# Performance work log

Measured on AMD Instinct MI355X. Metric: run time of the kernel, lower is better.

Reference implementation:

```python
import jax, jax.numpy as jnp
import numpy as np

VOCAB, EDIM, HDIM, ODIM = 100000, 128, 128, 10
BN_EPS = 1e-3  # keras BatchNormalization default epsilon


def _bn(x, gamma, beta, axes):
    # training-mode batch norm (batch statistics), as in a Keras training step
    m = jnp.mean(x, axis=axes, keepdims=True)
    v = jnp.var(x, axis=axes, keepdims=True)
    return gamma * (x - m) * jax.lax.rsqrt(v + BN_EPS) + beta


def _lstm_last(x, mask, W, U, b):
    # Keras LSTM, gate order [i, f, c, o]; masked steps carry state through.
    # x: [B,T,E], mask: [B,T] bool. Returns final hidden state [B,H].
    B, T, _ = x.shape
    H = U.shape[0]
    xg = jnp.einsum('bte,eg->btg', x, W) + b  # precomputed input projections [B,T,4H]

    def step(carry, inp):
        h, c = carry
        g, m = inp                      # g: [B,4H], m: [B]
        g = g + h @ U
        i, f, cc, o = jnp.split(g, 4, axis=-1)
        c_new = jax.nn.sigmoid(f) * c + jax.nn.sigmoid(i) * jnp.tanh(cc)
        h_new = jax.nn.sigmoid(o) * jnp.tanh(c_new)
        m = m[:, None]
        return (jnp.where(m, h_new, h), jnp.where(m, c_new, c)), None

    init = (jnp.zeros((B, H), x.dtype), jnp.zeros((B, H), x.dtype))
    (h, _), _ = jax.lax.scan(step, init, (xg.transpose(1, 0, 2), mask.T))
    return h


def setup_inputs() -> dict:
    key = jax.random.key(0)
    ks = jax.random.split(key, 12)
    s = 0.05
    ids = jax.random.randint(ks[0], (128, 1024), 0, VOCAB)
    return {
        'ids': ids,
        'embed_table': jax.random.normal(ks[1], (VOCAB, EDIM), jnp.float32) * s,
        'gamma1': jnp.ones((EDIM,), jnp.float32),
        'beta1': jnp.zeros((EDIM,), jnp.float32),
        'Wf': jax.random.normal(ks[2], (EDIM, 4 * HDIM), jnp.float32) * s,
        'Uf': jax.random.normal(ks[3], (HDIM, 4 * HDIM), jnp.float32) * s,
        'bf': jnp.zeros((4 * HDIM,), jnp.float32),
        'Wb': jax.random.normal(ks[4], (EDIM, 4 * HDIM), jnp.float32) * s,
        'Ub': jax.random.normal(ks[5], (HDIM, 4 * HDIM), jnp.float32) * s,
        'bb': jnp.zeros((4 * HDIM,), jnp.float32),
        'gamma2': jnp.ones((2 * HDIM,), jnp.float32),
        'beta2': jnp.zeros((2 * HDIM,), jnp.float32),
        'Wd': jax.random.normal(ks[6], (2 * HDIM, ODIM), jnp.float32) * s,
        'bd': jnp.zeros((ODIM,), jnp.float32),
    }


def reference(ids, embed_table, gamma1, beta1, Wf, Uf, bf, Wb, Ub, bb,
              gamma2, beta2, Wd, bd):
    mask = ids != 0                              # mask_zero=True
    x = embed_table[ids]                         # [B,T,E]
    x = _bn(x, gamma1, beta1, axes=(0, 1))
    h_fwd = _lstm_last(x, mask, Wf, Uf, bf)      # forward direction
    h_bwd = _lstm_last(x[:, ::-1], mask[:, ::-1], Wb, Ub, bb)  # go_backwards
    h = jnp.concatenate([h_fwd, h_bwd], axis=-1)  # merge_mode='concat' -> [B,2H]
    h = _bn(h, gamma2, beta2, axes=(0,))
    return jax.nn.softmax(h @ Wd + bd, axis=-1)
```

## Files before the change

kernel.cpp:

```cpp
#include <hip/hip_runtime.h>
#include <hip/hip_bf16.h>
#include <stdint.h>

#define VOCAB  100000
#define EDIM   128
#define HDIM   128
#define T_LEN  1024
#define BATCH  128
#define GDIM   512
#define NROWS  (BATCH*T_LEN)
#define BN_EPS 1e-3f

using short8 = __attribute__((ext_vector_type(8))) short;
using f32x4  = __attribute__((ext_vector_type(4))) float;

#define WS_SCALE  0u
#define WS_SHIFT  512u
#define WS_PSUM   1024u
#define WS_PSQ    (WS_PSUM + 524288u)
#define WS_HCAT   (WS_PSQ + 524288u)
#define WS_FRAGS  (WS_HCAT + 131072u)
#define WS_XN     (WS_FRAGS + 524288u)

__device__ __forceinline__ short f2bf(float f) {
    uint32_t u = __float_as_uint(f);
    return (short)((u + 0x7fffu + ((u >> 16) & 1u)) >> 16);
}

#define LOG2E 1.4426950408889634f
__device__ __forceinline__ float sigm2(float x) {
    return __builtin_amdgcn_rcpf(1.f + exp2f(x * (-LOG2E)));
}
__device__ __forceinline__ float tanh2(float x) {
    return 1.f - 2.f * __builtin_amdgcn_rcpf(1.f + exp2f(x * (2.f * LOG2E)));
}

#define BAR() asm volatile("s_waitcnt lgkmcnt(0)\n\ts_barrier" ::: "memory")

__global__ void k_bn1_partial(const int* __restrict__ ids,
                              const float* __restrict__ tab,
                              float* __restrict__ psum, float* __restrict__ psq) {
    __shared__ float ls[256], lq[256];
    int f = threadIdx.x & 127, rr = threadIdx.x >> 7;
    int r0 = blockIdx.x * 128;
    float s = 0.f, q = 0.f;
    for (int r = rr; r < 128; r += 2) {
        int id = ids[r0 + r];
        float v = tab[(size_t)id * EDIM + f];
        s += v; q += v * v;
    }
    ls[threadIdx.x] = s; lq[threadIdx.x] = q;
    __syncthreads();
    if (threadIdx.x < 128) {
        psum[blockIdx.x * 128 + f] = ls[f] + ls[f + 128];
        psq [blockIdx.x * 128 + f] = lq[f] + lq[f + 128];
    }
}

__global__ void k_bn1_final(const float* __restrict__ psum, const float* __restrict__ psq,
                            const float* __restrict__ gamma, const float* __restrict__ beta,
                            float* __restrict__ scale, float* __restrict__ shift) {
    int f = threadIdx.x;
    float s = 0.f, q = 0.f;
    for (int p = 0; p < 1024; ++p) { s += psum[p * 128 + f]; q += psq[p * 128 + f]; }
    const float inv_n = 1.0f / (float)NROWS;
    float m  = s * inv_n;
    float v  = q * inv_n - m * m;
    float sc = gamma[f] * rsqrtf(v + BN_EPS);
    scale[f] = sc;
    shift[f] = beta[f] - m * sc;
}

__global__ void k_embed_norm(const int* __restrict__ ids,
                             const float* __restrict__ tab,
                             const float* __restrict__ scale,
                             const float* __restrict__ shift,
                             short* __restrict__ xn) {
    int gid = blockIdx.x * blockDim.x + threadIdx.x;
    int row = gid >> 4, seg = gid & 15;
    int id  = ids[row];
    const float* src = tab + (size_t)id * EDIM + seg * 8;
    short8 out;
#pragma unroll
    for (int j = 0; j < 8; ++j) {
        float v = scale[seg * 8 + j] * src[j] + shift[seg * 8 + j];
        out[j] = f2bf(v);
    }
    *(short8*)(xn + (size_t)row * EDIM + seg * 8) = out;
}

__global__ void k_prepack(const float* __restrict__ Wf, const float* __restrict__ Uf,
                          const float* __restrict__ Wb, const float* __restrict__ Ub,
                          short* __restrict__ frags) {
    int gid = blockIdx.x * blockDim.x + threadIdx.x;
    int l  = gid & 63;
    int f  = (gid >> 6) & 31;
    int w  = (gid >> 11) & 7;
    int d  = gid >> 14;
    int s    = f >> 4;
    int gate = (f >> 2) & 3;
    int kc   = f & 3;
    const float* M = s ? (d ? Ub : Uf) : (d ? Wb : Wf);
    int rbase = 32 * kc + 8 * (l >> 4);
    int col   = 128 * gate + 16 * w + (l & 15);
    short8 out;
#pragma unroll
    for (int j = 0; j < 8; ++j) out[j] = f2bf(M[(size_t)(rbase + j) * GDIM + col]);
    *(short8*)(frags + (size_t)gid * 8) = out;
}

#define MFMA(A, B, C) __builtin_amdgcn_mfma_f32_16x16x32_bf16((A), (B), (C), 0, 0, 0)
#define S8(x) __builtin_bit_cast(short8, x)

__global__ void __launch_bounds__(512, 2)
k_lstm(const int* __restrict__ ids,
       const short* __restrict__ xn,
       const short* __restrict__ frags,
       const float* __restrict__ bf_, const float* __restrict__ bb_,
       float* __restrict__ hcat) {
    const int d   = blockIdx.x >> 7;
    const int b   = blockIdx.x & 127;
    const int tid = threadIdx.x;
    const int w   = tid >> 6, l = tid & 63, g = l >> 4, li = l & 15;

    __shared__ float xg_lds[2][16][512];
    __shared__ __align__(16) short h_s[2][HDIM];
    __shared__ unsigned char m_s[T_LEN];

    const short8* wsrc = (const short8*)frags + (size_t)(d * 8 + w) * 32 * 64 + l;

    short8 u00 = wsrc[(16+0)*64],  u01 = wsrc[(16+1)*64],  u02 = wsrc[(16+2)*64],  u03 = wsrc[(16+3)*64];
    short8 u10 = wsrc[(16+4)*64],  u11 = wsrc[(16+5)*64],  u12 = wsrc[(16+6)*64],  u13 = wsrc[(16+7)*64];
    short8 u20 = wsrc[(16+8)*64],  u21 = wsrc[(16+9)*64],  u22 = wsrc[(16+10)*64], u23 = wsrc[(16+11)*64];
    short8 u30 = wsrc[(16+12)*64], u31 = wsrc[(16+13)*64], u32 = wsrc[(16+14)*64], u33 = wsrc[(16+15)*64];

    short8 wq00 = wsrc[0*64],  wq01 = wsrc[1*64],  wq02 = wsrc[2*64],  wq03 = wsrc[3*64];
    short8 wq10 = wsrc[4*64],  wq11 = wsrc[5*64],  wq12 = wsrc[6*64],  wq13 = wsrc[7*64];
    short8 wq20 = wsrc[8*64],  wq21 = wsrc[9*64],  wq22 = wsrc[10*64], wq23 = wsrc[11*64];
    short8 wq30 = wsrc[12*64], wq31 = wsrc[13*64], wq32 = wsrc[14*64], wq33 = wsrc[15*64];

    const float* bias = d ? bb_ : bf_;
    const float bia0 = bias[0*128 + w*16 + li];
    const float bia1 = bias[1*128 + w*16 + li];
    const float bia2 = bias[2*128 + w*16 + li];
    const float bia3 = bias[3*128 + w*16 + li];

    {
        const int* idrow = ids + b * T_LEN;
        m_s[tid]       = idrow[tid] != 0;
        m_s[tid + 512] = idrow[tid + 512] != 0;
    }
    if (tid < HDIM) h_s[0][tid] = 0;
    float c_reg = 0.f, h_reg = 0.f;

    float* const xgw = &xg_lds[0][0][0] + w * 16 + li;

    uint4 ga0, ga1, ga2, ga3;
#define GATHER(C_) { \
        int s0_ = 16 * (C_) + li; \
        int p_  = d ? (T_LEN - 1 - s0_) : s0_; \
        const uint4* gb_ = (const uint4*)xn + (size_t)(b * T_LEN + p_) * 16; \
        ga0 = gb_[g]; ga1 = gb_[4 + g]; ga2 = gb_[8 + g]; ga3 = gb_[12 + g]; \
    }

#define XWGATE(GG, W0, W1, W2, W3, BIA, XGBASE) { \
        f32x4 ax = {(BIA), (BIA), (BIA), (BIA)}; \
        ax = MFMA(S8(ga0), W0, ax); \
        ax = MFMA(S8(ga1), W1, ax); \
        ax = MFMA(S8(ga2), W2, ax); \
        ax = MFMA(S8(ga3), W3, ax); \
        float* dst_ = (XGBASE) + (GG) * 128; \
        dst_[(4*g+0)*512] = ax[0]; dst_[(4*g+1)*512] = ax[1]; \
        dst_[(4*g+2)*512] = ax[2]; dst_[(4*g+3)*512] = ax[3]; \
    }

    GATHER(0);
    XWGATE(0, wq00, wq01, wq02, wq03, bia0, xgw);
    XWGATE(1, wq10, wq11, wq12, wq13, bia1, xgw);
    XWGATE(2, wq20, wq21, wq22, wq23, bia2, xgw);
    XWGATE(3, wq30, wq31, wq32, wq33, bia3, xgw);
    __syncthreads();

    float xa0, xa1, xa2, xa3, xb0, xb1, xb2, xb3;
    int   ma, mb;
    xa0 = xgw[0]; xa1 = xgw[128]; xa2 = xgw[256]; xa3 = xgw[384];
    ma  = m_s[d ? (T_LEN - 1) : 0];

    f32x4 a0 = {0.f,0.f,0.f,0.f}, a1 = {0.f,0.f,0.f,0.f};
    f32x4 a2 = {0.f,0.f,0.f,0.f}, a3 = {0.f,0.f,0.f,0.f};

#define STEP(J, XC0, XC1, XC2, XC3, XN0, XN1, XN2, XN3, MC, MN) { \
        const uint4* hp_ = (const uint4*)(h_s[(J) & 1]); \
        uint4 hf0 = hp_[g], hf1 = hp_[4 + g], hf2 = hp_[8 + g], hf3 = hp_[12 + g]; \
        a0[0] = (XC0); a1[0] = (XC1); a2[0] = (XC2); a3[0] = (XC3); \
        if (c < 63) { \
            if ((J) == 4) { wq00 = wsrc[0*64];  wq01 = wsrc[1*64];  wq02 = wsrc[2*64];  wq03 = wsrc[3*64];  } \
            if ((J) == 5) { wq10 = wsrc[4*64];  wq11 = wsrc[5*64];  wq12 = wsrc[6*64];  wq13 = wsrc[7*64];  } \
            if ((J) == 6) { wq20 = wsrc[8*64];  wq21 = wsrc[9*64];  wq22 = wsrc[10*64]; wq23 = wsrc[11*64]; } \
            if ((J) == 7) { wq30 = wsrc[12*64]; wq31 = wsrc[13*64]; wq32 = wsrc[14*64]; wq33 = wsrc[15*64]; } \
            if ((J) == 8)  XWGATE(0, wq00, wq01, wq02, wq03, bia0, xgw + ((c + 1) & 1) * 8192); \
            if ((J) == 9)  XWGATE(1, wq10, wq11, wq12, wq13, bia1, xgw + ((c + 1) & 1) * 8192); \
            if ((J) == 10) XWGATE(2, wq20, wq21, wq22, wq23, bia2, xgw + ((c + 1) & 1) * 8192); \
            if ((J) == 11) XWGATE(3, wq30, wq31, wq32, wq33, bia3, xgw + ((c + 1) & 1) * 8192); \
        } \
        a0 = MFMA(S8(hf0), u00, a0); a1 = MFMA(S8(hf0), u10, a1); \
        a2 = MFMA(S8(hf0), u20, a2); a3 = MFMA(S8(hf0), u30, a3); \
        a0 = MFMA(S8(hf1), u01, a0); a1 = MFMA(S8(hf1), u11, a1); \
        a2 = MFMA(S8(hf1), u21, a2); a3 = MFMA(S8(hf1), u31, a3); \
        a0 = MFMA(S8(hf2), u02, a0); a1 = MFMA(S8(hf2), u12, a1); \
        a2 = MFMA(S8(hf2), u22, a2); a3 = MFMA(S8(hf2), u32, a3); \
        a0 = MFMA(S8(hf3), u03, a0); a1 = MFMA(S8(hf3), u13, a1); \
        a2 = MFMA(S8(hf3), u23, a2); a3 = MFMA(S8(hf3), u33, a3); \
        if (!((c == 63) && ((J) == 15))) { \
            const float* rb_ = xgw + (((J) < 15) ? (c & 1) : ((c + 1) & 1)) * 8192 \
                                   + (((J) + 1) & 15) * 512; \
            XN0 = rb_[0]; XN1 = rb_[128]; XN2 = rb_[256]; XN3 = rb_[384]; \
            int sn_ = c * 16 + (J) + 1; \
            MN = m_s[d ? (T_LEN - 1 - sn_) : sn_]; \
        } \
        { \
            float gi = a0[0], gf = a1[0], gc = a2[0], go = a3[0]; \
            float si = sigm2(gi); \
            float sf = sigm2(gf); \
            float so = sigm2(go); \
            float tc = tanh2(gc); \
            float cn = sf * c_reg + si * tc; \
            float th = tanh2(cn); \
            float hn = so * th; \
            if (MC) { c_reg = cn; h_reg = hn; } \
            if (l < 16) h_s[((J) + 1) & 1][w * 16 + li] = f2bf(h_reg); \
        } \
        BAR(); \
    }

#pragma unroll 1
    for (int c = 0; c < 64; ++c) {
        if (c < 63) GATHER(c + 1);
        STEP(0,  xa0, xa1, xa2, xa3, xb0, xb1, xb2, xb3, ma, mb)
        STEP(1,  xb0, xb1, xb2, xb3, xa0, xa1, xa2, xa3, mb, ma)
        STEP(2,  xa0, xa1, xa2, xa3, xb0, xb1, xb2, xb3, ma, mb)
        STEP(3,  xb0, xb1, xb2, xb3, xa0, xa1, xa2, xa3, mb, ma)
        STEP(4,  xa0, xa1, xa2, xa3, xb0, xb1, xb2, xb3, ma, mb)
        STEP(5,  xb0, xb1, xb2, xb3, xa0, xa1, xa2, xa3, mb, ma)
        STEP(6,  xa0, xa1, xa2, xa3, xb0, xb1, xb2, xb3, ma, mb)
        STEP(7,  xb0, xb1, xb2, xb3, xa0, xa1, xa2, xa3, mb, ma)
        STEP(8,  xa0, xa1, xa2, xa3, xb0, xb1, xb2, xb3, ma, mb)
        STEP(9,  xb0, xb1, xb2, xb3, xa0, xa1, xa2, xa3, mb, ma)
        STEP(10, xa0, xa1, xa2, xa3, xb0, xb1, xb2, xb3, ma, mb)
        STEP(11, xb0, xb1, xb2, xb3, xa0, xa1, xa2, xa3, mb, ma)
        STEP(12, xa0, xa1, xa2, xa3, xb0, xb1, xb2, xb3, ma, mb)
        STEP(13, xb0, xb1, xb2, xb3, xa0, xa1, xa2, xa3, mb, ma)
        STEP(14, xa0, xa1, xa2, xa3, xb0, xb1, xb2, xb3, ma, mb)
        STEP(15, xb0, xb1, xb2, xb3, xa0, xa1, xa2, xa3, mb, ma)
    }

    if (l < 16) hcat[b * 256 + d * 128 + w * 16 + li] = h_reg;
}

__global__ void k_head(const float* __restrict__ hcat,
                       const float* __restrict__ gamma2, const float* __restrict__ beta2,
                       const float* __restrict__ Wd, const float* __restrict__ bd,
                       float* __restrict__ out) {
    __shared__ float sc_s[256], sh_s[256];
    __shared__ float logits[BATCH * 10];
    int tid = threadIdx.x;
    if (tid < 256) {
        float s = 0.f, q = 0.f;
        for (int bb = 0; bb < BATCH; ++bb) { float v = hcat[bb * 256 + tid]; s += v; q += v * v; }
        float m  = s / (float)BATCH;
        float v  = q / (float)BATCH - m * m;
        float sc = gamma2[tid] * rsqrtf(v + BN_EPS);
        sc_s[tid] = sc;
        sh_s[tid] = beta2[tid] - m * sc;
    }
    __syncthreads();
    {
        int bb = tid >> 3, oq = tid & 7;
        float acc0 = bd[oq], acc1 = (oq < 2) ? bd[8 + oq] : 0.f;
        for (int k = 0; k < 256; ++k) {
            float hv = sc_s[k] * hcat[bb * 256 + k] + sh_s[k];
            acc0 += hv * Wd[k * 10 + oq];
            if (oq < 2) acc1 += hv * Wd[k * 10 + 8 + oq];
        }
        logits[bb * 10 + oq] = acc0;
        if (oq < 2) logits[bb * 10 + 8 + oq] = acc1;
    }
    __syncthreads();
    if (tid < BATCH) {
        float lm = -1e30f;
#pragma unroll
        for (int o = 0; o < 10; ++o) lm = fmaxf(lm, logits[tid * 10 + o]);
        float e[10], s = 0.f;
#pragma unroll
        for (int o = 0; o < 10; ++o) { e[o] = __expf(logits[tid * 10 + o] - lm); s += e[o]; }
        float inv = __builtin_amdgcn_rcpf(s);
#pragma unroll
        for (int o = 0; o < 10; ++o) out[tid * 10 + o] = e[o] * inv;
    }
}

extern "C" void kernel_launch(void* const* d_in, const int* in_sizes, int n_in,
                              void* d_out, int out_size, void* d_ws, size_t ws_size,
                              hipStream_t stream) {
    const int*   ids = (const int*)  d_in[0];
    const float* tab = (const float*)d_in[1];
    const float* g1  = (const float*)d_in[2];
    const float* b1  = (const float*)d_in[3];
    const float* Wf  = (const float*)d_in[4];
    const float* Uf  = (const float*)d_in[5];
    const float* bfv = (const float*)d_in[6];
    const float* Wb  = (const float*)d_in[7];
    const float* Ub  = (const float*)d_in[8];
    const float* bbv = (const float*)d_in[9];
    const float* g2  = (const float*)d_in[10];
    const float* b2  = (const float*)d_in[11];
    const float* Wd  = (const float*)d_in[12];
    const float* bd  = (const float*)d_in[13];

    char*  ws    = (char*)d_ws;
    float* scale = (float*)(ws + WS_SCALE);
    float* shift = (float*)(ws + WS_SHIFT);
    float* psum  = (float*)(ws + WS_PSUM);
    float* psq   = (float*)(ws + WS_PSQ);
    float* hcat  = (float*)(ws + WS_HCAT);
    short* fragp = (short*)(ws + WS_FRAGS);
    short* xnp   = (short*)(ws + WS_XN);

    k_bn1_partial<<<1024, 256, 0, stream>>>(ids, tab, psum, psq);
    k_bn1_final  <<<1, 128, 0, stream>>>(psum, psq, g1, b1, scale, shift);
    k_embed_norm <<<8192, 256, 0, stream>>>(ids, tab, scale, shift, xnp);
    k_prepack    <<<128, 256, 0, stream>>>(Wf, Uf, Wb, Ub, fragp);
    k_lstm       <<<256, 512, 0, stream>>>(ids, xnp, fragp, bfv, bbv, hcat);
    k_head       <<<1, 1024, 0, stream>>>(hcat, g2, b2, Wd, bd, (float*)d_out);
}
```

Measured before the change: 678.4 us.

## Fold activation scales into LSTM weights, split MFMA chains, bit-pack masks

Pre-scales the gate weights and biases by -log2e (or 2log2e for the cell gate) during prepacking, so each sigmoid and tanh becomes a bare exp2 plus reciprocal. The recurrent MFMA chain is split into two independent accumulator chains, and the input projection is added after the MFMAs rather than seeded into them, which shortens the serial dependency on each step. Masks move from per-step LDS bytes to 64-bit ballot words built by a new kernel and read once per 16-step chunk. The xg LDS layout is made gate-interleaved so one vector load replaces four scalar loads, the per-chunk reload of W fragments is dropped, and bf16 conversion uses v_cvt_pk_bf16_f32. Rounding of the scaled weights to bf16 changes numerics slightly, and the mask words reuse the psum workspace region, which is safe only because the partial sums are consumed before the new kernel runs.

```diff
diff --git a/kernel.cpp b/kernel.cpp
--- a/kernel.cpp
+++ b/kernel.cpp
@@ -22,17 +22,12 @@
 #define WS_FRAGS  (WS_HCAT + 131072u)
 #define WS_XN     (WS_FRAGS + 524288u)
 
+#define SGI_K (-1.4426950408889634f)
+#define SGC_K ( 2.8853900817779268f)
+
 __device__ __forceinline__ short f2bf(float f) {
     uint32_t u = __float_as_uint(f);
     return (short)((u + 0x7fffu + ((u >> 16) & 1u)) >> 16);
-}
-
-#define LOG2E 1.4426950408889634f
-__device__ __forceinline__ float sigm2(float x) {
-    return __builtin_amdgcn_rcpf(1.f + exp2f(x * (-LOG2E)));
-}
-__device__ __forceinline__ float tanh2(float x) {
-    return 1.f - 2.f * __builtin_amdgcn_rcpf(1.f + exp2f(x * (2.f * LOG2E)));
 }
 
 #define BAR() asm volatile("s_waitcnt lgkmcnt(0)\n\ts_barrier" ::: "memory")
@@ -71,6 +66,12 @@
     shift[f] = beta[f] - m * sc;
 }
 
+__global__ void k_packmask(const int* __restrict__ ids, unsigned long long* __restrict__ mwords) {
+    int gid = blockIdx.x * 1024 + threadIdx.x;
+    unsigned long long bal = __ballot(ids[gid] != 0);
+    if ((threadIdx.x & 63) == 0) mwords[gid >> 6] = bal;
+}
+
 __global__ void k_embed_norm(const int* __restrict__ ids,
                              const float* __restrict__ tab,
                              const float* __restrict__ scale,
@@ -101,11 +102,12 @@
     int gate = (f >> 2) & 3;
     int kc   = f & 3;
     const float* M = s ? (d ? Ub : Uf) : (d ? Wb : Wf);
+    const float gs = (gate == 2) ? SGC_K : SGI_K;
     int rbase = 32 * kc + 8 * (l >> 4);
     int col   = 128 * gate + 16 * w + (l & 15);
     short8 out;
 #pragma unroll
-    for (int j = 0; j < 8; ++j) out[j] = f2bf(M[(size_t)(rbase + j) * GDIM + col]);
+    for (int j = 0; j < 8; ++j) out[j] = f2bf(gs * M[(size_t)(rbase + j) * GDIM + col]);
     *(short8*)(frags + (size_t)gid * 8) = out;
 }
 
@@ -113,9 +115,9 @@
 #define S8(x) __builtin_bit_cast(short8, x)
 
 __global__ void __launch_bounds__(512, 2)
-k_lstm(const int* __restrict__ ids,
-       const short* __restrict__ xn,
+k_lstm(const short* __restrict__ xn,
        const short* __restrict__ frags,
+       const unsigned long long* __restrict__ mwords,
        const float* __restrict__ bf_, const float* __restrict__ bb_,
        float* __restrict__ hcat) {
     const int d   = blockIdx.x >> 7;
@@ -125,35 +127,32 @@
 
     __shared__ float xg_lds[2][16][512];
     __shared__ __align__(16) short h_s[2][HDIM];
-    __shared__ unsigned char m_s[T_LEN];
+
+    float* const xgf = &xg_lds[0][0][0];
+    float* const xgr = xgf + (w * 16 + li) * 4;
 
     const short8* wsrc = (const short8*)frags + (size_t)(d * 8 + w) * 32 * 64 + l;
+
+    short8 wq00 = wsrc[0*64],  wq01 = wsrc[1*64],  wq02 = wsrc[2*64],  wq03 = wsrc[3*64];
+    short8 wq10 = wsrc[4*64],  wq11 = wsrc[5*64],  wq12 = wsrc[6*64],  wq13 = wsrc[7*64];
+    short8 wq20 = wsrc[8*64],  wq21 = wsrc[9*64],  wq22 = wsrc[10*64], wq23 = wsrc[11*64];
+    short8 wq30 = wsrc[12*64], wq31 = wsrc[13*64], wq32 = wsrc[14*64], wq33 = wsrc[15*64];
 
     short8 u00 = wsrc[(16+0)*64],  u01 = wsrc[(16+1)*64],  u02 = wsrc[(16+2)*64],  u03 = wsrc[(16+3)*64];
     short8 u10 = wsrc[(16+4)*64],  u11 = wsrc[(16+5)*64],  u12 = wsrc[(16+6)*64],  u13 = wsrc[(16+7)*64];
     short8 u20 = wsrc[(16+8)*64],  u21 = wsrc[(16+9)*64],  u22 = wsrc[(16+10)*64], u23 = wsrc[(16+11)*64];
     short8 u30 = wsrc[(16+12)*64], u31 = wsrc[(16+13)*64], u32 = wsrc[(16+14)*64], u33 = wsrc[(16+15)*64];
 
-    short8 wq00 = wsrc[0*64],  wq01 = wsrc[1*64],  wq02 = wsrc[2*64],  wq03 = wsrc[3*64];
-    short8 wq10 = wsrc[4*64],  wq11 = wsrc[5*64],  wq12 = wsrc[6*64],  wq13 = wsrc[7*64];
-    short8 wq20 = wsrc[8*64],  wq21 = wsrc[9*64],  wq22 = wsrc[10*64], wq23 = wsrc[11*64];
-    short8 wq30 = wsrc[12*64], wq31 = wsrc[13*64], wq32 = wsrc[14*64], wq33 = wsrc[15*64];
-
     const float* bias = d ? bb_ : bf_;
-    const float bia0 = bias[0*128 + w*16 + li];
-    const float bia1 = bias[1*128 + w*16 + li];
-    const float bia2 = bias[2*128 + w*16 + li];
-    const float bia3 = bias[3*128 + w*16 + li];
-
-    {
-        const int* idrow = ids + b * T_LEN;
-        m_s[tid]       = idrow[tid] != 0;
-        m_s[tid + 512] = idrow[tid + 512] != 0;
-    }
+    const float bia0 = bias[0*128 + w*16 + li] * SGI_K;
+    const float bia1 = bias[1*128 + w*16 + li] * SGI_K;
+    const float bia2 = bias[2*128 + w*16 + li] * SGC_K;
+    const float bia3 = bias[3*128 + w*16 + li] * SGI_K;
+
     if (tid < HDIM) h_s[0][tid] = 0;
     float c_reg = 0.f, h_reg = 0.f;
 
-    float* const xgw = &xg_lds[0][0][0] + w * 16 + li;
+    const f32x4 Z = {0.f, 0.f, 0.f, 0.f};
 
     uint4 ga0, ga1, ga2, ga3;
 #define GATHER(C_) { \
@@ -163,72 +162,76 @@
         ga0 = gb_[g]; ga1 = gb_[4 + g]; ga2 = gb_[8 + g]; ga3 = gb_[12 + g]; \
     }
 
-#define XWGATE(GG, W0, W1, W2, W3, BIA, XGBASE) { \
+#define XWGATE(GG, W0, W1, W2, W3, BIA, BUF) { \
         f32x4 ax = {(BIA), (BIA), (BIA), (BIA)}; \
         ax = MFMA(S8(ga0), W0, ax); \
         ax = MFMA(S8(ga1), W1, ax); \
         ax = MFMA(S8(ga2), W2, ax); \
         ax = MFMA(S8(ga3), W3, ax); \
-        float* dst_ = (XGBASE) + (GG) * 128; \
+        float* dst_ = xgf + (BUF) * 8192 + (w * 16 + li) * 4 + (GG); \
         dst_[(4*g+0)*512] = ax[0]; dst_[(4*g+1)*512] = ax[1]; \
         dst_[(4*g+2)*512] = ax[2]; dst_[(4*g+3)*512] = ax[3]; \
     }
 
     GATHER(0);
-    XWGATE(0, wq00, wq01, wq02, wq03, bia0, xgw);
-    XWGATE(1, wq10, wq11, wq12, wq13, bia1, xgw);
-    XWGATE(2, wq20, wq21, wq22, wq23, bia2, xgw);
-    XWGATE(3, wq30, wq31, wq32, wq33, bia3, xgw);
+    XWGATE(0, wq00, wq01, wq02, wq03, bia0, 0);
+    XWGATE(1, wq10, wq11, wq12, wq13, bia1, 0);
+    XWGATE(2, wq20, wq21, wq22, wq23, bia2, 0);
+    XWGATE(3, wq30, wq31, wq32, wq33, bia3, 0);
     __syncthreads();
 
     float xa0, xa1, xa2, xa3, xb0, xb1, xb2, xb3;
-    int   ma, mb;
-    xa0 = xgw[0]; xa1 = xgw[128]; xa2 = xgw[256]; xa3 = xgw[384];
-    ma  = m_s[d ? (T_LEN - 1) : 0];
-
-    f32x4 a0 = {0.f,0.f,0.f,0.f}, a1 = {0.f,0.f,0.f,0.f};
-    f32x4 a2 = {0.f,0.f,0.f,0.f}, a3 = {0.f,0.f,0.f,0.f};
-
-#define STEP(J, XC0, XC1, XC2, XC3, XN0, XN1, XN2, XN3, MC, MN) { \
+    {
+        const f32x4 xv0 = *(const f32x4*)(xgr);
+        xa0 = xv0[0]; xa1 = xv0[1]; xa2 = xv0[2]; xa3 = xv0[3];
+    }
+
+#define STEP(J, XC0, XC1, XC2, XC3, XN0, XN1, XN2, XN3) { \
         const uint4* hp_ = (const uint4*)(h_s[(J) & 1]); \
         uint4 hf0 = hp_[g], hf1 = hp_[4 + g], hf2 = hp_[8 + g], hf3 = hp_[12 + g]; \
-        a0[0] = (XC0); a1[0] = (XC1); a2[0] = (XC2); a3[0] = (XC3); \
         if (c < 63) { \
-            if ((J) == 4) { wq00 = wsrc[0*64];  wq01 = wsrc[1*64];  wq02 = wsrc[2*64];  wq03 = wsrc[3*64];  } \
-            if ((J) == 5) { wq10 = wsrc[4*64];  wq11 = wsrc[5*64];  wq12 = wsrc[6*64];  wq13 = wsrc[7*64];  } \
-            if ((J) == 6) { wq20 = wsrc[8*64];  wq21 = wsrc[9*64];  wq22 = wsrc[10*64]; wq23 = wsrc[11*64]; } \
-            if ((J) == 7) { wq30 = wsrc[12*64]; wq31 = wsrc[13*64]; wq32 = wsrc[14*64]; wq33 = wsrc[15*64]; } \
-            if ((J) == 8)  XWGATE(0, wq00, wq01, wq02, wq03, bia0, xgw + ((c + 1) & 1) * 8192); \
-            if ((J) == 9)  XWGATE(1, wq10, wq11, wq12, wq13, bia1, xgw + ((c + 1) & 1) * 8192); \
-            if ((J) == 10) XWGATE(2, wq20, wq21, wq22, wq23, bia2, xgw + ((c + 1) & 1) * 8192); \
-            if ((J) == 11) XWGATE(3, wq30, wq31, wq32, wq33, bia3, xgw + ((c + 1) & 1) * 8192); \
+            if ((J) == 8)  XWGATE(0, wq00, wq01, wq02, wq03, bia0, ((c + 1) & 1)); \
+            if ((J) == 9)  XWGATE(1, wq10, wq11, wq12, wq13, bia1, ((c + 1) & 1)); \
+            if ((J) == 10) XWGATE(2, wq20, wq21, wq22, wq23, bia2, ((c + 1) & 1)); \
+            if ((J) == 11) XWGATE(3, wq30, wq31, wq32, wq33, bia3, ((c + 1) & 1)); \
         } \
-        a0 = MFMA(S8(hf0), u00, a0); a1 = MFMA(S8(hf0), u10, a1); \
-        a2 = MFMA(S8(hf0), u20, a2); a3 = MFMA(S8(hf0), u30, a3); \
-        a0 = MFMA(S8(hf1), u01, a0); a1 = MFMA(S8(hf1), u11, a1); \
-        a2 = MFMA(S8(hf1), u21, a2); a3 = MFMA(S8(hf1), u31, a3); \
-        a0 = MFMA(S8(hf2), u02, a0); a1 = MFMA(S8(hf2), u12, a1); \
-        a2 = MFMA(S8(hf2), u22, a2); a3 = MFMA(S8(hf2), u32, a3); \
-        a0 = MFMA(S8(hf3), u03, a0); a1 = MFMA(S8(hf3), u13, a1); \
-        a2 = MFMA(S8(hf3), u23, a2); a3 = MFMA(S8(hf3), u33, a3); \
+        f32x4 p0 = MFMA(S8(hf0), u00, Z); \
+        f32x4 p1 = MFMA(S8(hf0), u10, Z); \
+        f32x4 p2 = MFMA(S8(hf0), u20, Z); \
+        f32x4 p3 = MFMA(S8(hf0), u30, Z); \
+        f32x4 q0 = MFMA(S8(hf2), u02, Z); \
+        f32x4 q1 = MFMA(S8(hf2), u12, Z); \
+        f32x4 q2 = MFMA(S8(hf2), u22, Z); \
+        f32x4 q3 = MFMA(S8(hf2), u32, Z); \
+        p0 = MFMA(S8(hf1), u01, p0); \
+        p1 = MFMA(S8(hf1), u11, p1); \
+        p2 = MFMA(S8(hf1), u21, p2); \
+        p3 = MFMA(S8(hf1), u31, p3); \
+        q0 = MFMA(S8(hf3), u03, q0); \
+        q1 = MFMA(S8(hf3), u13, q1); \
+        q2 = MFMA(S8(hf3), u23, q2); \
+        q3 = MFMA(S8(hf3), u33, q3); \
         if (!((c == 63) && ((J) == 15))) { \
-            const float* rb_ = xgw + (((J) < 15) ? (c & 1) : ((c + 1) & 1)) * 8192 \
-                                   + (((J) + 1) & 15) * 512; \
-            XN0 = rb_[0]; XN1 = rb_[128]; XN2 = rb_[256]; XN3 = rb_[384]; \
-            int sn_ = c * 16 + (J) + 1; \
-            MN = m_s[d ? (T_LEN - 1 - sn_) : sn_]; \
+            const f32x4 xv_ = *(const f32x4*)(xgr + (((J) < 15) ? (c & 1) : ((c + 1) & 1)) * 8192 \
+                                                  + (((J) + 1) & 15) * 512); \
+            XN0 = xv_[0]; XN1 = xv_[1]; XN2 = xv_[2]; XN3 = xv_[3]; \
         } \
         { \
-            float gi = a0[0], gf = a1[0], gc = a2[0], go = a3[0]; \
-            float si = sigm2(gi); \
-            float sf = sigm2(gf); \
-            float so = sigm2(go); \
-            float tc = tanh2(gc); \
-            float cn = sf * c_reg + si * tc; \
-            float th = tanh2(cn); \
+            float gi = (XC0) + (p0[0] + q0[0]); \
+            float gf = (XC1) + (p1[0] + q1[0]); \
+            float gc = (XC2) + (p2[0] + q2[0]); \
+            float go = (XC3) + (p3[0] + q3[0]); \
+            float si = __builtin_amdgcn_rcpf(1.f + exp2f(gi)); \
+            float sf = __builtin_amdgcn_rcpf(1.f + exp2f(gf)); \
+            float so = __builtin_amdgcn_rcpf(1.f + exp2f(go)); \
+            float tc = __builtin_fmaf(-2.f, __builtin_amdgcn_rcpf(1.f + exp2f(gc)), 1.f); \
+            float cn = __builtin_fmaf(sf, c_reg, si * tc); \
+            float th = __builtin_fmaf(-2.f, __builtin_amdgcn_rcpf(1.f + exp2f(cn * SGC_K)), 1.f); \
             float hn = so * th; \
-            if (MC) { c_reg = cn; h_reg = hn; } \
-            if (l < 16) h_s[((J) + 1) & 1][w * 16 + li] = f2bf(h_reg); \
+            if (mb & (1u << (J))) { c_reg = cn; h_reg = hn; } \
+            uint32_t pk_; \
+            asm("v_cvt_pk_bf16_f32 %0, %1, %2" : "=v"(pk_) : "v"(h_reg), "v"(h_reg)); \
+            if (l < 16) h_s[((J) + 1) & 1][w * 16 + li] = (short)pk_; \
         } \
         BAR(); \
     }
@@ -236,22 +239,26 @@
 #pragma unroll 1
     for (int c = 0; c < 64; ++c) {
         if (c < 63) GATHER(c + 1);
-        STEP(0,  xa0, xa1, xa2, xa3, xb0, xb1, xb2, xb3, ma, mb)
-        STEP(1,  xb0, xb1, xb2, xb3, xa0, xa1, xa2, xa3, mb, ma)
-        STEP(2,  xa0, xa1, xa2, xa3, xb0, xb1, xb2, xb3, ma, mb)
-        STEP(3,  xb0, xb1, xb2, xb3, xa0, xa1, xa2, xa3, mb, ma)
-        STEP(4,  xa0, xa1, xa2, xa3, xb0, xb1, xb2, xb3, ma, mb)
-        STEP(5,  xb0, xb1, xb2, xb3, xa0, xa1, xa2, xa3, mb, ma)
-        STEP(6,  xa0, xa1, xa2, xa3, xb0, xb1, xb2, xb3, ma, mb)
-        STEP(7,  xb0, xb1, xb2, xb3, xa0, xa1, xa2, xa3, mb, ma)
-        STEP(8,  xa0, xa1, xa2, xa3, xb0, xb1, xb2, xb3, ma, mb)
-        STEP(9,  xb0, xb1, xb2, xb3, xa0, xa1, xa2, xa3, mb, ma)
-        STEP(10, xa0, xa1, xa2, xa3, xb0, xb1, xb2, xb3, ma, mb)
-        STEP(11, xb0, xb1, xb2, xb3, xa0, xa1, xa2, xa3, mb, ma)
-        STEP(12, xa0, xa1, xa2, xa3, xb0, xb1, xb2, xb3, ma, mb)
-        STEP(13, xb0, xb1, xb2, xb3, xa0, xa1, xa2, xa3, mb, ma)
-        STEP(14, xa0, xa1, xa2, xa3, xb0, xb1, xb2, xb3, ma, mb)
-        STEP(15, xb0, xb1, xb2, xb3, xa0, xa1, xa2, xa3, mb, ma)
+        int cc_ = d ? 63 - c : c;
+        unsigned long long mw_ = mwords[(size_t)b * 16 + (cc_ >> 2)];
+        uint32_t mb = (uint32_t)(mw_ >> ((cc_ & 3) * 16)) & 0xFFFFu;
+        if (d) mb = __builtin_bitreverse32(mb) >> 16;
+        STEP(0,  xa0, xa1, xa2, xa3, xb0, xb1, xb2, xb3)
+        STEP(1,  xb0, xb1, xb2, xb3, xa0, xa1, xa2, xa3)
+        STEP(2,  xa0, xa1, xa2, xa3, xb0, xb1, xb2, xb3)
+        STEP(3,  xb0, xb1, xb2, xb3, xa0, xa1, xa2, xa3)
+        STEP(4,  xa0, xa1, xa2, xa3, xb0, xb1, xb2, xb3)
+        STEP(5,  xb0, xb1, xb2, xb3, xa0, xa1, xa2, xa3)
+        STEP(6,  xa0, xa1, xa2, xa3, xb0, xb1, xb2, xb3)
+        STEP(7,  xb0, xb1, xb2, xb3, xa0, xa1, xa2, xa3)
+        STEP(8,  xa0, xa1, xa2, xa3, xb0, xb1, xb2, xb3)
+        STEP(9,  xb0, xb1, xb2, xb3, xa0, xa1, xa2, xa3)
+        STEP(10, xa0, xa1, xa2, xa3, xb0, xb1, xb2, xb3)
+        STEP(11, xb0, xb1, xb2, xb3, xa0, xa1, xa2, xa3)
+        STEP(12, xa0, xa1, xa2, xa3, xb0, xb1, xb2, xb3)
+        STEP(13, xb0, xb1, xb2, xb3, xa0, xa1, xa2, xa3)
+        STEP(14, xa0, xa1, xa2, xa3, xb0, xb1, xb2, xb3)
+        STEP(15, xb0, xb1, xb2, xb3, xa0, xa1, xa2, xa3)
     }
 
     if (l < 16) hcat[b * 256 + d * 128 + w * 16 + li] = h_reg;
@@ -325,11 +332,13 @@
     float* hcat  = (float*)(ws + WS_HCAT);
     short* fragp = (short*)(ws + WS_FRAGS);
     short* xnp   = (short*)(ws + WS_XN);
+    unsigned long long* mwords = (unsigned long long*)(ws + WS_PSUM);
 
     k_bn1_partial<<<1024, 256, 0, stream>>>(ids, tab, psum, psq);
     k_bn1_final  <<<1, 128, 0, stream>>>(psum, psq, g1, b1, scale, shift);
+    k_packmask   <<<128, 1024, 0, stream>>>(ids, mwords);
     k_embed_norm <<<8192, 256, 0, stream>>>(ids, tab, scale, shift, xnp);
     k_prepack    <<<128, 256, 0, stream>>>(Wf, Uf, Wb, Ub, fragp);
-    k_lstm       <<<256, 512, 0, stream>>>(ids, xnp, fragp, bfv, bbv, hcat);
+    k_lstm       <<<256, 512, 0, stream>>>(xnp, fragp, mwords, bfv, bbv, hcat);
     k_head       <<<1, 1024, 0, stream>>>(hcat, g2, b2, Wd, bd, (float*)d_out);
 }
```

Measured after the change: 645.2 us. 4.9% less time.
